# Kernel tuning notes

Measured on AMD Instinct MI355X. Metric: run time of the kernel, lower is better.

The kernel has to match this reference:

```python
import jax, jax.numpy as jnp
import numpy as np

N = 50000   # nodes per graph
E = 800000  # edges per graph
FIN = 128   # node_features
H = 4       # heads
C = 32      # out channels per head (hidden_dim // heads)
HID = H * C # 128
FE = 16     # edge_features
B = 8       # graphs in batch
NEG_SLOPE = 0.2


def setup_inputs() -> dict:
    key = jax.random.key(0)
    ks = jax.random.split(key, 30)
    f32 = jnp.float32
    inp = {
        'x_a': jax.random.normal(ks[0], (N, FIN), f32),
        'edge_index_a': jax.random.randint(ks[1], (2, E), 0, N),
        'edge_attr_a': jax.random.normal(ks[2], (E, FE), f32),
        'batch_a': jnp.sort(jax.random.randint(ks[3], (N,), 0, B)),
        'x_b': jax.random.normal(ks[4], (N, FIN), f32),
        'edge_index_b': jax.random.randint(ks[5], (2, E), 0, N),
        'edge_attr_b': jax.random.normal(ks[6], (E, FE), f32),
        'batch_b': jnp.sort(jax.random.randint(ks[7], (N,), 0, B)),
    }
    def p(i, shape, s=0.05):
        return jax.random.normal(ks[i], shape, f32) * s
    # GAT layer 1 (in FIN -> H*C)
    inp['W1l'] = p(8, (FIN, HID)); inp['b1l'] = jnp.zeros((HID,), f32)
    inp['W1r'] = p(9, (FIN, HID)); inp['b1r'] = jnp.zeros((HID,), f32)
    inp['W1e'] = p(10, (FE, HID))
    inp['att1'] = p(11, (H, C))
    inp['bias1'] = jnp.zeros((HID,), f32)
    # GAT layer 2 (in HID -> H*C)
    inp['W2l'] = p(12, (HID, HID)); inp['b2l'] = jnp.zeros((HID,), f32)
    inp['W2r'] = p(13, (HID, HID)); inp['b2r'] = jnp.zeros((HID,), f32)
    inp['W2e'] = p(14, (FE, HID))
    inp['att2'] = p(15, (H, C))
    inp['bias2'] = jnp.zeros((HID,), f32)
    # fc head: Linear(4*HID, HID) -> ReLU -> Linear(HID, 1)
    inp['Wf1'] = p(16, (4 * HID, HID)); inp['bf1'] = jnp.zeros((HID,), f32)
    inp['Wf2'] = p(17, (HID, 1)); inp['bf2'] = jnp.zeros((1,), f32)
    return inp


def gatv2(x, edge_index, edge_attr, Wl, bl, Wr, br, We, att, bias):
    """GATv2Conv (concat=True), eval mode (no dropout)."""
    src, dst = edge_index[0], edge_index[1]
    n = x.shape[0]
    xl = (x @ Wl + bl).reshape(n, H, C)  # source transform
    xr = (x @ Wr + br).reshape(n, H, C)  # target transform
    # per-edge pre-activation: x_j + x_i + edge_emb  -> [E, H, C]
    m = xl[src] + xr[dst] + (edge_attr @ We).reshape(-1, H, C)
    logits = jnp.einsum('ehc,hc->eh', jax.nn.leaky_relu(m, NEG_SLOPE), att)  # [E, H]
    # scatter-softmax over incoming edges of each destination node
    lmax = jax.ops.segment_max(logits, dst, num_segments=n)
    lmax = jnp.where(jnp.isfinite(lmax), lmax, 0.0)
    ex = jnp.exp(logits - lmax[dst])
    denom = jax.ops.segment_sum(ex, dst, num_segments=n)
    alpha = ex / (denom[dst] + 1e-16)  # [E, H]
    out = jax.ops.segment_sum(alpha[:, :, None] * xl[src], dst, num_segments=n)  # [N, H, C]
    return out.reshape(n, HID) + bias


def encode(x, edge_index, edge_attr, batch,
           W1l, b1l, W1r, b1r, W1e, att1, bias1,
           W2l, b2l, W2r, b2r, W2e, att2, bias2):
    h = jax.nn.elu(gatv2(x, edge_index, edge_attr, W1l, b1l, W1r, b1r, W1e, att1, bias1))
    h = jax.nn.elu(gatv2(h, edge_index, edge_attr, W2l, b2l, W2r, b2r, W2e, att2, bias2))
    cnt = jnp.clip(jax.ops.segment_sum(jnp.ones((h.shape[0],), h.dtype), batch, num_segments=B), 1.0)
    h_mean = jax.ops.segment_sum(h, batch, num_segments=B) / cnt[:, None]
    h_max = jax.ops.segment_max(h, batch, num_segments=B)
    h_max = jnp.where(jnp.isfinite(h_max), h_max, 0.0)
    return jnp.concatenate([h_mean, h_max], axis=-1)  # [B, 2*HID]


def reference(x_a, edge_index_a, edge_attr_a, batch_a,
              x_b, edge_index_b, edge_attr_b, batch_b,
              W1l, b1l, W1r, b1r, W1e, att1, bias1,
              W2l, b2l, W2r, b2r, W2e, att2, bias2,
              Wf1, bf1, Wf2, bf2):
    emb_a = encode(x_a, edge_index_a, edge_attr_a, batch_a,
                   W1l, b1l, W1r, b1r, W1e, att1, bias1,
                   W2l, b2l, W2r, b2r, W2e, att2, bias2)
    emb_b = encode(x_b, edge_index_b, edge_attr_b, batch_b,
                   W1l, b1l, W1r, b1r, W1e, att1, bias1,
                   W2l, b2l, W2r, b2r, W2e, att2, bias2)
    combined = jnp.concatenate([emb_a, emb_b], axis=-1)  # [B, 4*HID]
    hidden = jax.nn.relu(combined @ Wf1 + bf1)
    dominance = jax.nn.sigmoid(hidden @ Wf2 + bf2).squeeze(-1)  # [B]
    return dominance
```

## Files before the change

### kernel.cpp

```cpp
#include <hip/hip_runtime.h>
#include <hip/hip_fp16.h>

#define NN 50000
#define NE 800000
#define HIDD 128
#define FEAT_E 16
#define NGRAPH 8
#define CAP 64

typedef __attribute__((ext_vector_type(2))) _Float16 half2_t;
typedef __attribute__((ext_vector_type(8))) _Float16 half8_t;
typedef __attribute__((ext_vector_type(4))) float floatx4;


__device__ __forceinline__ unsigned int fenc(float f) {
  unsigned int u = __float_as_uint(f);
  return (u & 0x80000000u) ? ~u : (u | 0x80000000u);
}
__device__ __forceinline__ float fdec(unsigned int u) {
  if (u == 0u) return 0.0f;
  float f = (u & 0x80000000u) ? __uint_as_float(u & 0x7fffffffu)
                              : __uint_as_float(~u);
  return __builtin_isfinite(f) ? f : 0.0f;
}

__device__ __forceinline__ half8_t splat8(_Float16 v) {
  return (half8_t){v, v, v, v, v, v, v, v};
}
__device__ __forceinline__ half8_t hmax8(half8_t a, half8_t b) {
#if __has_builtin(__builtin_elementwise_max)
  return __builtin_elementwise_max(a, b);
#else
  half8_t r;
#pragma unroll
  for (int i = 0; i < 8; ++i) r[i] = a[i] > b[i] ? a[i] : b[i];
  return r;
#endif
}
__device__ __forceinline__ float dot_att(half8_t lk, half2_t t01, half2_t t23,
                                         half2_t t45, half2_t t67) {
#if __has_builtin(__builtin_amdgcn_fdot2)
  float p = __builtin_amdgcn_fdot2((half2_t){lk[0], lk[1]}, t01, 0.f, false);
  p = __builtin_amdgcn_fdot2((half2_t){lk[2], lk[3]}, t23, p, false);
  p = __builtin_amdgcn_fdot2((half2_t){lk[4], lk[5]}, t45, p, false);
  p = __builtin_amdgcn_fdot2((half2_t){lk[6], lk[7]}, t67, p, false);
  return p;
#else
  float p = 0.f;
  p += (float)lk[0] * (float)t01[0] + (float)lk[1] * (float)t01[1];
  p += (float)lk[2] * (float)t23[0] + (float)lk[3] * (float)t23[1];
  p += (float)lk[4] * (float)t45[0] + (float)lk[5] * (float)t45[1];
  p += (float)lk[6] * (float)t67[0] + (float)lk[7] * (float)t67[1];
  return p;
#endif
}

__global__ void prep_wt_k(const float* __restrict__ Wl, const float* __restrict__ Wr,
                          _Float16* __restrict__ wtg) {
  const int r = blockIdx.x & 127;
  const int which = blockIdx.x >> 7;
  const int k = threadIdx.x;
  const float* W = which ? Wr : Wl;
  const int oc_src = (r & 15) * 8 + (r >> 4);
  const int col = k ^ ((r & 7) << 3);
  wtg[(which * 128 + r) * 128 + col] = (_Float16)W[k * 128 + oc_src];
}

__device__ __forceinline__ half8_t load_a8(const _Float16* p) {
  return *(const half8_t*)p;
}
__device__ __forceinline__ half8_t load_a8(const float* p) {
  const float4 f0 = *(const float4*)p;
  const float4 f1 = *(const float4*)(p + 4);
  return (half8_t){(_Float16)f0.x, (_Float16)f0.y, (_Float16)f0.z, (_Float16)f0.w,
                   (_Float16)f1.x, (_Float16)f1.y, (_Float16)f1.z, (_Float16)f1.w};
}

template <typename TIN>
__global__ __launch_bounds__(256) void node_linear_mfma_k(
    const TIN* __restrict__ x, const _Float16* __restrict__ wtg,
    const float* __restrict__ bl, const float* __restrict__ br,
    _Float16* __restrict__ xl16, _Float16* __restrict__ xr16) {
  __shared__ _Float16 wt[128 * 128];
  const int tid = threadIdx.x;
  const int which = blockIdx.y;
  const _Float16* wsrc = wtg + which * (128 * 128);
  const float* bias128 = which ? br : bl;
  _Float16* out = which ? xr16 : xl16;
  {
    const half8_t* src = (const half8_t*)wsrc;
    half8_t* dstl = (half8_t*)wt;
#pragma unroll
    for (int it = 0; it < 8; ++it)
      dstl[it * 256 + tid] = src[it * 256 + tid];
  }
  __syncthreads();

  const int wv = tid >> 6, lane = tid & 63;
  const int arow = lane & 15, kq = lane >> 4;
  const int nbase = blockIdx.x * 64 + wv * 16;
  int nload = nbase + arow;
  if (nload >= NN) nload = NN - 1;
  floatx4 acc[8];
#pragma unroll
  for (int t = 0; t < 8; ++t) acc[t] = (floatx4){0.f, 0.f, 0.f, 0.f};
#pragma unroll
  for (int kb = 0; kb < 4; ++kb) {
    const half8_t a = load_a8(x + (size_t)nload * 128 + kb * 32 + kq * 8);
    const int colbase = (kb * 32 + kq * 8) ^ ((arow & 7) << 3);
#pragma unroll
    for (int t = 0; t < 8; ++t) {
      const half8_t b = *(const half8_t*)&wt[(t * 16 + arow) * 128 + colbase];
      acc[t] = __builtin_amdgcn_mfma_f32_16x16x32_f16(a, b, acc[t], 0, 0, 0);
    }
  }
  const float4 bv0 = *(const float4*)&bias128[arow * 8];
  const float4 bv1 = *(const float4*)&bias128[arow * 8 + 4];
  const float bv[8] = {bv0.x, bv0.y, bv0.z, bv0.w, bv1.x, bv1.y, bv1.z, bv1.w};
#pragma unroll
  for (int i = 0; i < 4; ++i) {
    const int n = nbase + kq * 4 + i;
    if (n < NN) {
      half8_t v;
#pragma unroll
      for (int t = 0; t < 8; ++t) v[t] = (_Float16)(acc[t][i] + bv[t]);
      *(half8_t*)(out + (size_t)n * 128 + arow * 8) = v;
    }
  }
}

__global__ void build_k(const int* __restrict__ src, const int* __restrict__ dst,
                        const float* __restrict__ eattr,
                        int* __restrict__ cnt, int2* __restrict__ bpair,
                        _Float16* __restrict__ eatt16) {
  const int e = blockIdx.x * blockDim.x + threadIdx.x;
  if (e >= NE) return;
  const float4* ea = (const float4*)(eattr + (size_t)e * FEAT_E);
  const float4 a0 = ea[0], a1 = ea[1], a2 = ea[2], a3 = ea[3];
  half8_t h0 = {(_Float16)a0.x, (_Float16)a0.y, (_Float16)a0.z, (_Float16)a0.w,
                (_Float16)a1.x, (_Float16)a1.y, (_Float16)a1.z, (_Float16)a1.w};
  half8_t h1 = {(_Float16)a2.x, (_Float16)a2.y, (_Float16)a2.z, (_Float16)a2.w,
                (_Float16)a3.x, (_Float16)a3.y, (_Float16)a3.z, (_Float16)a3.w};
  half8_t* eo = (half8_t*)(eatt16 + (size_t)e * FEAT_E);
  eo[0] = h0; eo[1] = h1;
  const int d = dst[e];
  const int pos = atomicAdd(&cnt[d], 1);
  if (pos < CAP) bpair[(size_t)d * CAP + pos] = make_int2(src[e], e);
}

__global__ __launch_bounds__(256) void node_gat_fused_k(
    const _Float16* __restrict__ xl16, const _Float16* __restrict__ xr16,
    const _Float16* __restrict__ eatt16,
    const int2* __restrict__ bpair, const int* __restrict__ cnt,
    const float* __restrict__ We, const float* __restrict__ att,
    const float* __restrict__ bias, _Float16* __restrict__ hout) {
  __shared__ half8_t WeS[FEAT_E][16];
  const int tid = threadIdx.x;
  {
    const int f = tid >> 4, q = tid & 15;
    const float4 w0 = ((const float4*)We)[f * 32 + q * 2];
    const float4 w1 = ((const float4*)We)[f * 32 + q * 2 + 1];
    WeS[f][q] = (half8_t){(_Float16)w0.x, (_Float16)w0.y, (_Float16)w0.z, (_Float16)w0.w,
                          (_Float16)w1.x, (_Float16)w1.y, (_Float16)w1.z, (_Float16)w1.w};
  }
  __syncthreads();

  const int wave = tid >> 6, lane = tid & 63;
  const int slot = lane >> 4, l16 = lane & 15;
  const int d = blockIdx.x * 4 + wave;

  const float4 af0 = ((const float4*)att)[l16 * 2];
  const float4 af1 = ((const float4*)att)[l16 * 2 + 1];
  const half2_t at01 = {(_Float16)af0.x, (_Float16)af0.y};
  const half2_t at23 = {(_Float16)af0.z, (_Float16)af0.w};
  const half2_t at45 = {(_Float16)af1.x, (_Float16)af1.y};
  const half2_t at67 = {(_Float16)af1.z, (_Float16)af1.w};

  const half8_t xrh = *(const half8_t*)(xr16 + (size_t)d * HIDD + l16 * 8);

  int deg = cnt[d];
  deg = deg < CAP ? deg : CAP;
  const int2* bp = bpair + (size_t)d * CAP;

  float acc0 = 0.f, acc1 = 0.f, acc2 = 0.f, acc3 = 0.f;
  float acc4 = 0.f, acc5 = 0.f, acc6 = 0.f, acc7 = 0.f;
  float den = 0.f;

#define FINISH_EDGE(XL, EM)                                              \
  {                                                                      \
    half8_t m_ = ((XL) + xrh) + (EM);                                    \
    half8_t lk_ = hmax8(m_, m_ * splat8((_Float16)0.2f));                \
    float p_ = dot_att(lk_, at01, at23, at45, at67);                     \
    p_ += __shfl_xor(p_, 1);                                             \
    p_ += __shfl_xor(p_, 2);                                             \
    const float w_ = __expf(p_);                                         \
    den += w_;                                                           \
    acc0 = fmaf(w_, (float)(XL)[0], acc0);                               \
    acc1 = fmaf(w_, (float)(XL)[1], acc1);                               \
    acc2 = fmaf(w_, (float)(XL)[2], acc2);                               \
    acc3 = fmaf(w_, (float)(XL)[3], acc3);                               \
    acc4 = fmaf(w_, (float)(XL)[4], acc4);                               \
    acc5 = fmaf(w_, (float)(XL)[5], acc5);                               \
    acc6 = fmaf(w_, (float)(XL)[6], acc6);                               \
    acc7 = fmaf(w_, (float)(XL)[7], acc7);                               \
  }

  int j = slot;
  for (; j + 4 < deg; j += 8) {
    const int2 p0 = bp[j];
    const int2 p1 = bp[j + 4];
    const half8_t x0 = *(const half8_t*)(xl16 + (unsigned)p0.x * 128u + l16 * 8);
    const half8_t x1 = *(const half8_t*)(xl16 + (unsigned)p1.x * 128u + l16 * 8);
    const half8_t a0 = *(const half8_t*)(eatt16 + (unsigned)p0.y * 16u);
    const half8_t b0 = *(const half8_t*)(eatt16 + (unsigned)p0.y * 16u + 8u);
    const half8_t a1 = *(const half8_t*)(eatt16 + (unsigned)p1.y * 16u);
    const half8_t b1 = *(const half8_t*)(eatt16 + (unsigned)p1.y * 16u + 8u);
    half8_t em0 = {}, em1 = {};
#pragma unroll
    for (int f = 0; f < 8; ++f) {
      const half8_t wf = WeS[f][l16];
      em0 += splat8(a0[f]) * wf;
      em1 += splat8(a1[f]) * wf;
    }
#pragma unroll
    for (int f = 0; f < 8; ++f) {
      const half8_t wf = WeS[8 + f][l16];
      em0 += splat8(b0[f]) * wf;
      em1 += splat8(b1[f]) * wf;
    }
    FINISH_EDGE(x0, em0)
    FINISH_EDGE(x1, em1)
  }
  if (j < deg) {
    const int2 p0 = bp[j];
    const half8_t x0 = *(const half8_t*)(xl16 + (unsigned)p0.x * 128u + l16 * 8);
    const half8_t a0 = *(const half8_t*)(eatt16 + (unsigned)p0.y * 16u);
    const half8_t b0 = *(const half8_t*)(eatt16 + (unsigned)p0.y * 16u + 8u);
    half8_t em0 = {};
#pragma unroll
    for (int f = 0; f < 8; ++f) em0 += splat8(a0[f]) * WeS[f][l16];
#pragma unroll
    for (int f = 0; f < 8; ++f) em0 += splat8(b0[f]) * WeS[8 + f][l16];
    FINISH_EDGE(x0, em0)
  }
#undef FINISH_EDGE

#define RED(A) A += __shfl_xor(A, 16); A += __shfl_xor(A, 32);
  RED(acc0) RED(acc1) RED(acc2) RED(acc3)
  RED(acc4) RED(acc5) RED(acc6) RED(acc7)
  RED(den)
#undef RED
  if (slot == 0) {
    const float inv = 1.f / (den + 1e-16f);
    const float4 b0 = ((const float4*)bias)[l16 * 2];
    const float4 b1 = ((const float4*)bias)[l16 * 2 + 1];
    float o0 = fmaf(acc0, inv, b0.x), o1 = fmaf(acc1, inv, b0.y);
    float o2 = fmaf(acc2, inv, b0.z), o3 = fmaf(acc3, inv, b0.w);
    float o4 = fmaf(acc4, inv, b1.x), o5 = fmaf(acc5, inv, b1.y);
    float o6 = fmaf(acc6, inv, b1.z), o7 = fmaf(acc7, inv, b1.w);
    o0 = o0 > 0.f ? o0 : expm1f(o0);  o1 = o1 > 0.f ? o1 : expm1f(o1);
    o2 = o2 > 0.f ? o2 : expm1f(o2);  o3 = o3 > 0.f ? o3 : expm1f(o3);
    o4 = o4 > 0.f ? o4 : expm1f(o4);  o5 = o5 > 0.f ? o5 : expm1f(o5);
    o6 = o6 > 0.f ? o6 : expm1f(o6);  o7 = o7 > 0.f ? o7 : expm1f(o7);
    half8_t ho = {(_Float16)o0, (_Float16)o1, (_Float16)o2, (_Float16)o3,
                  (_Float16)o4, (_Float16)o5, (_Float16)o6, (_Float16)o7};
    *(half8_t*)(hout + (size_t)d * HIDD + l16 * 8) = ho;
  }
}

__global__ void pool_k(const _Float16* __restrict__ h, const int* __restrict__ batch,
                       float* __restrict__ gsum, unsigned int* __restrict__ gmax,
                       float* __restrict__ gcnt) {
  __shared__ float ssum[NGRAPH][HIDD];
  __shared__ float smax[NGRAPH][HIDD];
  __shared__ float scnt[NGRAPH];
  const int t = threadIdx.x;
#pragma unroll
  for (int g = 0; g < NGRAPH; ++g) {
    ssum[g][t] = 0.f;
    smax[g][t] = -3.0e38f;
  }
  if (t < NGRAPH) scnt[t] = 0.f;
  __syncthreads();
  const int n0 = blockIdx.x * 64;
  const int nEnd = (n0 + 64 < NN) ? (n0 + 64) : NN;
  unsigned int seen = 0;
  for (int n = n0; n < nEnd; ++n) {
    const int g = batch[n];
    seen |= 1u << g;
    const float v = (float)h[(size_t)n * HIDD + t];
    ssum[g][t] += v;
    smax[g][t] = fmaxf(smax[g][t], v);
    if (t == 0) scnt[g] += 1.f;
  }
  __syncthreads();
  for (int g = 0; g < NGRAPH; ++g) {
    if (seen & (1u << g)) {
      atomicAdd(&gsum[g * HIDD + t], ssum[g][t]);
      atomicMax(&gmax[g * HIDD + t], fenc(smax[g][t]));
      if (t == 0) atomicAdd(&gcnt[g], scnt[g]);
    }
  }
}

__global__ void head_k(const float* __restrict__ suma, const unsigned int* __restrict__ maxa,
                       const float* __restrict__ cnta,
                       const float* __restrict__ sumb, const unsigned int* __restrict__ maxb,
                       const float* __restrict__ cntb,
                       const float* __restrict__ Wf1, const float* __restrict__ bf1,
                       const float* __restrict__ Wf2, const float* __restrict__ bf2,
                       float* __restrict__ out) {
  __shared__ float c[4 * HIDD];
  __shared__ float red[HIDD];
  const int g = blockIdx.x, t = threadIdx.x;
  const float ca = fmaxf(cnta[g], 1.f), cb = fmaxf(cntb[g], 1.f);
  c[t]            = suma[g * HIDD + t] / ca;
  c[HIDD + t]     = fdec(maxa[g * HIDD + t]);
  c[2 * HIDD + t] = sumb[g * HIDD + t] / cb;
  c[3 * HIDD + t] = fdec(maxb[g * HIDD + t]);
  __syncthreads();
  float acc = bf1[t];
  for (int i = 0; i < 4 * HIDD; ++i)
    acc = fmaf(c[i], Wf1[(size_t)i * HIDD + t], acc);
  acc = fmaxf(acc, 0.f);
  red[t] = acc * Wf2[t];
  __syncthreads();
  for (int s2 = 64; s2 > 0; s2 >>= 1) {
    if (t < s2) red[t] += red[t + s2];
    __syncthreads();
  }
  if (t == 0) out[g] = 1.f / (1.f + expf(-(red[0] + bf2[0])));
}

extern "C" void kernel_launch(void* const* d_in, const int* in_sizes, int n_in,
                              void* d_out, int out_size, void* d_ws, size_t ws_size,
                              hipStream_t stream) {
  (void)in_sizes; (void)n_in; (void)out_size; (void)ws_size;
  const float* xA    = (const float*)d_in[0];
  const int*   eiA   = (const int*)  d_in[1];
  const float* eaA   = (const float*)d_in[2];
  const int*   batA  = (const int*)  d_in[3];
  const float* xB    = (const float*)d_in[4];
  const int*   eiB   = (const int*)  d_in[5];
  const float* eaB   = (const float*)d_in[6];
  const int*   batB  = (const int*)  d_in[7];
  const float* W1l   = (const float*)d_in[8];
  const float* b1l   = (const float*)d_in[9];
  const float* W1r   = (const float*)d_in[10];
  const float* b1r   = (const float*)d_in[11];
  const float* W1e   = (const float*)d_in[12];
  const float* att1  = (const float*)d_in[13];
  const float* bias1 = (const float*)d_in[14];
  const float* W2l   = (const float*)d_in[15];
  const float* b2l   = (const float*)d_in[16];
  const float* W2r   = (const float*)d_in[17];
  const float* b2r   = (const float*)d_in[18];
  const float* W2e   = (const float*)d_in[19];
  const float* att2  = (const float*)d_in[20];
  const float* bias2 = (const float*)d_in[21];
  const float* Wf1   = (const float*)d_in[22];
  const float* bf1   = (const float*)d_in[23];
  const float* Wf2   = (const float*)d_in[24];
  const float* bf2   = (const float*)d_in[25];

  char* ws = (char*)d_ws;
  size_t off = 0;
  auto alloc = [&](size_t bytes) -> void* {
    void* p = ws + off;
    off += (bytes + 255) & ~(size_t)255;
    return p;
  };
  _Float16* h16    = (_Float16*)alloc((size_t)NN * HIDD * 2);
  _Float16* xl16   = (_Float16*)alloc((size_t)NN * HIDD * 2);
  _Float16* xr16   = (_Float16*)alloc((size_t)NN * HIDD * 2);
  int2*     bpair  = (int2*)    alloc((size_t)NN * CAP * 8);
  _Float16* eatt16 = (_Float16*)alloc((size_t)NE * FEAT_E * 2);
  int*      cnt    = (int*)     alloc((size_t)NN * 4);
  _Float16* wtg1   = (_Float16*)alloc(2 * 128 * 128 * 2);
  _Float16* wtg2   = (_Float16*)alloc(2 * 128 * 128 * 2);
  const size_t poolStart = off;
  float*        psumA = (float*)alloc(NGRAPH * HIDD * 4);
  unsigned int* pmaxA = (unsigned int*)alloc(NGRAPH * HIDD * 4);
  float*        pcntA = (float*)alloc(NGRAPH * 4);
  float*        psumB = (float*)alloc(NGRAPH * HIDD * 4);
  unsigned int* pmaxB = (unsigned int*)alloc(NGRAPH * HIDD * 4);
  float*        pcntB = (float*)alloc(NGRAPH * 4);
  const size_t poolBytes = off - poolStart;

  const float* xs[2]   = {xA, xB};
  const int*   eis[2]  = {eiA, eiB};
  const float* eas[2]  = {eaA, eaB};
  const int*   bats[2] = {batA, batB};
  float*        psums[2] = {psumA, psumB};
  unsigned int* pmaxs[2] = {pmaxA, pmaxB};
  float*        pcnts[2] = {pcntA, pcntB};

  hipMemsetAsync(psumA, 0, poolBytes, stream);
  prep_wt_k<<<256, 128, 0, stream>>>(W1l, W1r, wtg1);
  prep_wt_k<<<256, 128, 0, stream>>>(W2l, W2r, wtg2);

  for (int g = 0; g < 2; ++g) {
    const int* src = eis[g];
    const int* dst = eis[g] + NE;
    hipMemsetAsync(cnt, 0, (size_t)NN * 4, stream);
    build_k<<<NE / 256, 256, 0, stream>>>(src, dst, eas[g], cnt, bpair, eatt16);
    node_linear_mfma_k<float><<<dim3((NN + 63) / 64, 2), 256, 0, stream>>>(
        xs[g], wtg1, b1l, b1r, xl16, xr16);
    node_gat_fused_k<<<NN / 4, 256, 0, stream>>>(xl16, xr16, eatt16, bpair, cnt,
                                                 W1e, att1, bias1, h16);
    node_linear_mfma_k<_Float16><<<dim3((NN + 63) / 64, 2), 256, 0, stream>>>(
        h16, wtg2, b2l, b2r, xl16, xr16);
    node_gat_fused_k<<<NN / 4, 256, 0, stream>>>(xl16, xr16, eatt16, bpair, cnt,
                                                 W2e, att2, bias2, h16);
    pool_k<<<(NN + 63) / 64, 128, 0, stream>>>(h16, bats[g], psums[g], pmaxs[g], pcnts[g]);
  }
  head_k<<<NGRAPH, 128, 0, stream>>>(psumA, pmaxA, pcntA, psumB, pmaxB, pcntB,
                                     Wf1, bf1, Wf2, bf2, (float*)d_out);
}
```

Measured before the change: 853.9 us.

## Replace capped per-node edge buckets with CSR built by count-scan-place

Builds a true CSR adjacency with a count kernel, a single-block prefix scan, and a placement kernel. The placement kernel writes source indices and fp16 edge attributes in destination-sorted order. The GAT aggregation then reads edge attributes contiguously instead of gathering them by edge id, and drops the degree cap. The cost is two extra launches per graph, including a serial single-block scan, plus scattered writes during placement.

```diff
diff --git a/kernel.cpp b/kernel.cpp
--- a/kernel.cpp
+++ b/kernel.cpp
@@ -6,12 +6,10 @@
 #define HIDD 128
 #define FEAT_E 16
 #define NGRAPH 8
-#define CAP 64
 
 typedef __attribute__((ext_vector_type(2))) _Float16 half2_t;
 typedef __attribute__((ext_vector_type(8))) _Float16 half8_t;
 typedef __attribute__((ext_vector_type(4))) float floatx4;
-
 
 __device__ __forceinline__ unsigned int fenc(float f) {
   unsigned int u = __float_as_uint(f);
@@ -129,29 +127,64 @@
   }
 }
 
-__global__ void build_k(const int* __restrict__ src, const int* __restrict__ dst,
-                        const float* __restrict__ eattr,
-                        int* __restrict__ cnt, int2* __restrict__ bpair,
-                        _Float16* __restrict__ eatt16) {
+__global__ void count_k(const int* __restrict__ dst, int* __restrict__ cnt) {
+  const int e = blockIdx.x * blockDim.x + threadIdx.x;
+  if (e >= NE) return;
+  atomicAdd(&cnt[dst[e]], 1);
+}
+
+__global__ __launch_bounds__(1024) void scan_k(const int* __restrict__ cnt,
+                                               int* __restrict__ offs,
+                                               int* __restrict__ cursor) {
+  __shared__ int part[1024];
+  const int t = threadIdx.x;
+  const int base = t * 49;
+  int s = 0;
+  for (int i = 0; i < 49; ++i) {
+    const int idx = base + i;
+    if (idx < NN) s += cnt[idx];
+  }
+  part[t] = s;
+  __syncthreads();
+  for (int o = 1; o < 1024; o <<= 1) {
+    const int v = (t >= o) ? part[t - o] : 0;
+    __syncthreads();
+    part[t] += v;
+    __syncthreads();
+  }
+  int run = (t == 0) ? 0 : part[t - 1];
+  for (int i = 0; i < 49; ++i) {
+    const int idx = base + i;
+    if (idx < NN) {
+      offs[idx] = run;
+      cursor[idx] = run;
+      run += cnt[idx];
+    }
+  }
+  if (t == 0) offs[NN] = NE;
+}
+
+__global__ void place_k(const int* __restrict__ src, const int* __restrict__ dst,
+                        const float* __restrict__ eattr, int* __restrict__ cursor,
+                        int* __restrict__ srcB, _Float16* __restrict__ eattB) {
   const int e = blockIdx.x * blockDim.x + threadIdx.x;
   if (e >= NE) return;
   const float4* ea = (const float4*)(eattr + (size_t)e * FEAT_E);
   const float4 a0 = ea[0], a1 = ea[1], a2 = ea[2], a3 = ea[3];
-  half8_t h0 = {(_Float16)a0.x, (_Float16)a0.y, (_Float16)a0.z, (_Float16)a0.w,
-                (_Float16)a1.x, (_Float16)a1.y, (_Float16)a1.z, (_Float16)a1.w};
-  half8_t h1 = {(_Float16)a2.x, (_Float16)a2.y, (_Float16)a2.z, (_Float16)a2.w,
-                (_Float16)a3.x, (_Float16)a3.y, (_Float16)a3.z, (_Float16)a3.w};
-  half8_t* eo = (half8_t*)(eatt16 + (size_t)e * FEAT_E);
+  const half8_t h0 = {(_Float16)a0.x, (_Float16)a0.y, (_Float16)a0.z, (_Float16)a0.w,
+                      (_Float16)a1.x, (_Float16)a1.y, (_Float16)a1.z, (_Float16)a1.w};
+  const half8_t h1 = {(_Float16)a2.x, (_Float16)a2.y, (_Float16)a2.z, (_Float16)a2.w,
+                      (_Float16)a3.x, (_Float16)a3.y, (_Float16)a3.z, (_Float16)a3.w};
+  const int pos = atomicAdd(&cursor[dst[e]], 1);
+  srcB[pos] = src[e];
+  half8_t* eo = (half8_t*)(eattB + (size_t)pos * FEAT_E);
   eo[0] = h0; eo[1] = h1;
-  const int d = dst[e];
-  const int pos = atomicAdd(&cnt[d], 1);
-  if (pos < CAP) bpair[(size_t)d * CAP + pos] = make_int2(src[e], e);
 }
 
 __global__ __launch_bounds__(256) void node_gat_fused_k(
     const _Float16* __restrict__ xl16, const _Float16* __restrict__ xr16,
-    const _Float16* __restrict__ eatt16,
-    const int2* __restrict__ bpair, const int* __restrict__ cnt,
+    const _Float16* __restrict__ eattB, const int* __restrict__ srcB,
+    const int* __restrict__ offs,
     const float* __restrict__ We, const float* __restrict__ att,
     const float* __restrict__ bias, _Float16* __restrict__ hout) {
   __shared__ half8_t WeS[FEAT_E][16];
@@ -177,23 +210,20 @@
   const half2_t at67 = {(_Float16)af1.z, (_Float16)af1.w};
 
   const half8_t xrh = *(const half8_t*)(xr16 + (size_t)d * HIDD + l16 * 8);
-
-  int deg = cnt[d];
-  deg = deg < CAP ? deg : CAP;
-  const int2* bp = bpair + (size_t)d * CAP;
+  const int o0 = offs[d], o1 = offs[d + 1];
 
   float acc0 = 0.f, acc1 = 0.f, acc2 = 0.f, acc3 = 0.f;
   float acc4 = 0.f, acc5 = 0.f, acc6 = 0.f, acc7 = 0.f;
   float den = 0.f;
 
-#define FINISH_EDGE(XL, EM)                                              \
+#define FINISH_EDGE(XL, EM, V)                                           \
   {                                                                      \
     half8_t m_ = ((XL) + xrh) + (EM);                                    \
     half8_t lk_ = hmax8(m_, m_ * splat8((_Float16)0.2f));                \
     float p_ = dot_att(lk_, at01, at23, at45, at67);                     \
     p_ += __shfl_xor(p_, 1);                                             \
     p_ += __shfl_xor(p_, 2);                                             \
-    const float w_ = __expf(p_);                                         \
+    const float w_ = (V) ? __expf(p_) : 0.f;                             \
     den += w_;                                                           \
     acc0 = fmaf(w_, (float)(XL)[0], acc0);                               \
     acc1 = fmaf(w_, (float)(XL)[1], acc1);                               \
@@ -205,16 +235,17 @@
     acc7 = fmaf(w_, (float)(XL)[7], acc7);                               \
   }
 
-  int j = slot;
-  for (; j + 4 < deg; j += 8) {
-    const int2 p0 = bp[j];
-    const int2 p1 = bp[j + 4];
-    const half8_t x0 = *(const half8_t*)(xl16 + (unsigned)p0.x * 128u + l16 * 8);
-    const half8_t x1 = *(const half8_t*)(xl16 + (unsigned)p1.x * 128u + l16 * 8);
-    const half8_t a0 = *(const half8_t*)(eatt16 + (unsigned)p0.y * 16u);
-    const half8_t b0 = *(const half8_t*)(eatt16 + (unsigned)p0.y * 16u + 8u);
-    const half8_t a1 = *(const half8_t*)(eatt16 + (unsigned)p1.y * 16u);
-    const half8_t b1 = *(const half8_t*)(eatt16 + (unsigned)p1.y * 16u + 8u);
+  for (int j = o0 + slot * 2; j < o1; j += 8) {
+    const bool v1 = (j + 1) < o1;
+    const int j1 = v1 ? j + 1 : j;
+    const int s0 = srcB[j];
+    const int s1 = srcB[j1];
+    const half8_t x0 = *(const half8_t*)(xl16 + (unsigned)s0 * 128u + l16 * 8);
+    const half8_t x1 = *(const half8_t*)(xl16 + (unsigned)s1 * 128u + l16 * 8);
+    const half8_t a0 = *(const half8_t*)(eattB + (unsigned)j * 16u);
+    const half8_t b0 = *(const half8_t*)(eattB + (unsigned)j * 16u + 8u);
+    const half8_t a1 = *(const half8_t*)(eattB + (unsigned)j1 * 16u);
+    const half8_t b1 = *(const half8_t*)(eattB + (unsigned)j1 * 16u + 8u);
     half8_t em0 = {}, em1 = {};
 #pragma unroll
     for (int f = 0; f < 8; ++f) {
@@ -228,20 +259,8 @@
       em0 += splat8(b0[f]) * wf;
       em1 += splat8(b1[f]) * wf;
     }
-    FINISH_EDGE(x0, em0)
-    FINISH_EDGE(x1, em1)
-  }
-  if (j < deg) {
-    const int2 p0 = bp[j];
-    const half8_t x0 = *(const half8_t*)(xl16 + (unsigned)p0.x * 128u + l16 * 8);
-    const half8_t a0 = *(const half8_t*)(eatt16 + (unsigned)p0.y * 16u);
-    const half8_t b0 = *(const half8_t*)(eatt16 + (unsigned)p0.y * 16u + 8u);
-    half8_t em0 = {};
-#pragma unroll
-    for (int f = 0; f < 8; ++f) em0 += splat8(a0[f]) * WeS[f][l16];
-#pragma unroll
-    for (int f = 0; f < 8; ++f) em0 += splat8(b0[f]) * WeS[8 + f][l16];
-    FINISH_EDGE(x0, em0)
+    FINISH_EDGE(x0, em0, true)
+    FINISH_EDGE(x1, em1, v1)
   }
 #undef FINISH_EDGE
 
@@ -254,16 +273,16 @@
     const float inv = 1.f / (den + 1e-16f);
     const float4 b0 = ((const float4*)bias)[l16 * 2];
     const float4 b1 = ((const float4*)bias)[l16 * 2 + 1];
-    float o0 = fmaf(acc0, inv, b0.x), o1 = fmaf(acc1, inv, b0.y);
-    float o2 = fmaf(acc2, inv, b0.z), o3 = fmaf(acc3, inv, b0.w);
-    float o4 = fmaf(acc4, inv, b1.x), o5 = fmaf(acc5, inv, b1.y);
-    float o6 = fmaf(acc6, inv, b1.z), o7 = fmaf(acc7, inv, b1.w);
-    o0 = o0 > 0.f ? o0 : expm1f(o0);  o1 = o1 > 0.f ? o1 : expm1f(o1);
-    o2 = o2 > 0.f ? o2 : expm1f(o2);  o3 = o3 > 0.f ? o3 : expm1f(o3);
-    o4 = o4 > 0.f ? o4 : expm1f(o4);  o5 = o5 > 0.f ? o5 : expm1f(o5);
-    o6 = o6 > 0.f ? o6 : expm1f(o6);  o7 = o7 > 0.f ? o7 : expm1f(o7);
-    half8_t ho = {(_Float16)o0, (_Float16)o1, (_Float16)o2, (_Float16)o3,
-                  (_Float16)o4, (_Float16)o5, (_Float16)o6, (_Float16)o7};
+    float o0f = fmaf(acc0, inv, b0.x), o1f = fmaf(acc1, inv, b0.y);
+    float o2f = fmaf(acc2, inv, b0.z), o3f = fmaf(acc3, inv, b0.w);
+    float o4f = fmaf(acc4, inv, b1.x), o5f = fmaf(acc5, inv, b1.y);
+    float o6f = fmaf(acc6, inv, b1.z), o7f = fmaf(acc7, inv, b1.w);
+    o0f = o0f > 0.f ? o0f : expm1f(o0f);  o1f = o1f > 0.f ? o1f : expm1f(o1f);
+    o2f = o2f > 0.f ? o2f : expm1f(o2f);  o3f = o3f > 0.f ? o3f : expm1f(o3f);
+    o4f = o4f > 0.f ? o4f : expm1f(o4f);  o5f = o5f > 0.f ? o5f : expm1f(o5f);
+    o6f = o6f > 0.f ? o6f : expm1f(o6f);  o7f = o7f > 0.f ? o7f : expm1f(o7f);
+    half8_t ho = {(_Float16)o0f, (_Float16)o1f, (_Float16)o2f, (_Float16)o3f,
+                  (_Float16)o4f, (_Float16)o5f, (_Float16)o6f, (_Float16)o7f};
     *(half8_t*)(hout + (size_t)d * HIDD + l16 * 8) = ho;
   }
 }
@@ -373,9 +392,11 @@
   _Float16* h16    = (_Float16*)alloc((size_t)NN * HIDD * 2);
   _Float16* xl16   = (_Float16*)alloc((size_t)NN * HIDD * 2);
   _Float16* xr16   = (_Float16*)alloc((size_t)NN * HIDD * 2);
-  int2*     bpair  = (int2*)    alloc((size_t)NN * CAP * 8);
-  _Float16* eatt16 = (_Float16*)alloc((size_t)NE * FEAT_E * 2);
+  int*      srcB   = (int*)     alloc((size_t)NE * 4);
+  _Float16* eattB  = (_Float16*)alloc((size_t)NE * FEAT_E * 2);
   int*      cnt    = (int*)     alloc((size_t)NN * 4);
+  int*      offs   = (int*)     alloc((size_t)(NN + 1) * 4);
+  int*      cursor = (int*)     alloc((size_t)NN * 4);
   _Float16* wtg1   = (_Float16*)alloc(2 * 128 * 128 * 2);
   _Float16* wtg2   = (_Float16*)alloc(2 * 128 * 128 * 2);
   const size_t poolStart = off;
@@ -403,14 +424,16 @@
     const int* src = eis[g];
     const int* dst = eis[g] + NE;
     hipMemsetAsync(cnt, 0, (size_t)NN * 4, stream);
-    build_k<<<NE / 256, 256, 0, stream>>>(src, dst, eas[g], cnt, bpair, eatt16);
+    count_k<<<NE / 256, 256, 0, stream>>>(dst, cnt);
+    scan_k<<<1, 1024, 0, stream>>>(cnt, offs, cursor);
+    place_k<<<NE / 256, 256, 0, stream>>>(src, dst, eas[g], cursor, srcB, eattB);
     node_linear_mfma_k<float><<<dim3((NN + 63) / 64, 2), 256, 0, stream>>>(
         xs[g], wtg1, b1l, b1r, xl16, xr16);
-    node_gat_fused_k<<<NN / 4, 256, 0, stream>>>(xl16, xr16, eatt16, bpair, cnt,
+    node_gat_fused_k<<<NN / 4, 256, 0, stream>>>(xl16, xr16, eattB, srcB, offs,
                                                  W1e, att1, bias1, h16);
     node_linear_mfma_k<_Float16><<<dim3((NN + 63) / 64, 2), 256, 0, stream>>>(
         h16, wtg2, b2l, b2r, xl16, xr16);
-    node_gat_fused_k<<<NN / 4, 256, 0, stream>>>(xl16, xr16, eatt16, bpair, cnt,
+    node_gat_fused_k<<<NN / 4, 256, 0, stream>>>(xl16, xr16, eattB, srcB, offs,
                                                  W2e, att2, bias2, h16);
     pool_k<<<(NN + 63) / 64, 128, 0, stream>>>(h16, bats[g], psums[g], pmaxs[g], pcnts[g]);
   }
```

Measured after the change: 1.142 ms. 1.34x slower.
